# Performance work log

Hardware: AMD Instinct MI355X
Metric: run time of the kernel (lower is better)

## Reference

```python
import jax, jax.numpy as jnp
import numpy as np

B = 131072
F = 512

def setup_inputs() -> dict:
    key = jax.random.key(0)
    kx, kq = jax.random.split(key)
    x = jax.random.normal(kx, (B, F), dtype=jnp.float32)
    # Q param: xavier-normal init, then strictly-lower-triangular entries zeroed
    # (mask = tril(ones, diagonal=-1); Q.masked_fill_(mask, 0)).
    std = float(np.sqrt(2.0 / (F + F)))
    Q = jax.random.normal(kq, (F, F), dtype=jnp.float32) * std
    Q = jnp.triu(Q)  # zero strictly-lower triangle, keep diagonal
    return {"x": x, "Q": Q}

def reference(x, Q):
    # Original: diag(x @ Q @ x.T).view(-1, 1).
    # Equivalent per-row bilinear form, avoiding the [B, B] intermediate:
    # out[b] = sum_f sum_g x[b,f] Q[f,g] x[b,g]
    xQ = x @ Q                           # [B, F]
    out = jnp.sum(xQ * x, axis=1, keepdims=True)  # [B, 1]
    return out
```

## Files before the change

### kernel.cpp

```cpp
#include <hip/hip_runtime.h>
#include <hip/hip_bf16.h>

typedef __bf16 bf16_t;
typedef __bf16 bf16x8 __attribute__((ext_vector_type(8)));
typedef __bf16 bf16x4 __attribute__((ext_vector_type(4)));
typedef float f32x4 __attribute__((ext_vector_type(4)));

#define FDIM 512
#define BM 64
#define NTHR 512

__global__ void qtrans_kernel(const float* __restrict__ Q, bf16_t* __restrict__ Qt) {
    __shared__ float t[32][33];
    int tx = threadIdx.x & 31;
    int ty = threadIdx.x >> 5;
    int f0 = blockIdx.x * 32;
    int g0 = blockIdx.y * 32;
#pragma unroll
    for (int i = 0; i < 4; ++i)
        t[ty + 8 * i][tx] = Q[(size_t)(f0 + ty + 8 * i) * FDIM + g0 + tx];
    __syncthreads();
#pragma unroll
    for (int i = 0; i < 4; ++i)
        Qt[(size_t)(g0 + ty + 8 * i) * FDIM + f0 + tx] = (bf16_t)t[tx][ty + 8 * i];
}

__global__ __launch_bounds__(NTHR, 4) void bilinear_kernel(
    const float* __restrict__ x, const bf16_t* __restrict__ Qt,
    float* __restrict__ out)
{
    __shared__ bf16_t xs[BM * FDIM];
    __shared__ float rsum[8][BM];

    const int tid = threadIdx.x;
    const size_t blk = (size_t)blockIdx.x * BM;
    const float4* xin = (const float4*)(x + blk * FDIM);

#pragma unroll 1
    for (int it = 0; it < 4; ++it) {
        float4 vv[4];
#pragma unroll
        for (int j = 0; j < 4; ++j) vv[j] = xin[(it * 4 + j) * NTHR + tid];
#pragma unroll
        for (int j = 0; j < 4; ++j) {
            int e = ((it * 4 + j) * NTHR + tid) * 4;
            int row = e >> 9;
            int se = e ^ ((row & 7) << 3);
            bf16x4 b;
            b[0] = (bf16_t)vv[j].x; b[1] = (bf16_t)vv[j].y;
            b[2] = (bf16_t)vv[j].z; b[3] = (bf16_t)vv[j].w;
            *(bf16x4*)(xs + se) = b;
        }
        __builtin_amdgcn_sched_barrier(0);
    }
    __syncthreads();

    const int w   = tid >> 6;
    const int l   = tid & 63;
    const int col = l & 15;
    const int kg  = l >> 4;

    float rs[4][4];
#pragma unroll
    for (int m = 0; m < 4; ++m)
#pragma unroll
        for (int j = 0; j < 4; ++j) rs[m][j] = 0.0f;

#pragma unroll 1
    for (int pi = 0; pi < 4; ++pi) {
        const int p  = (pi < 2) ? w : (15 - w);
        const int h  = pi & 1;
        const int c0 = p * 32 + h * 16;
        const int nk = p + 1;

        f32x4 acc[4];
#pragma unroll
        for (int m = 0; m < 4; ++m)
#pragma unroll
            for (int j = 0; j < 4; ++j) acc[m][j] = 0.0f;

        const bf16_t* qb = Qt + (size_t)(c0 + col) * FDIM + kg * 8;
        bf16x8 b0 = *(const bf16x8*)(qb);

        for (int ks = 0; ks < nk; ++ks) {
            bf16x8 nb = b0;
            if (ks + 1 < nk) nb = *(const bf16x8*)(qb + (ks + 1) * 32);
            bf16x8 a[4];
#pragma unroll
            for (int m = 0; m < 4; ++m) {
                int r = m * 16 + col;
                int e = (r * FDIM + ks * 32 + kg * 8) ^ ((r & 7) << 3);
                a[m] = *(const bf16x8*)(xs + e);
            }
#pragma unroll
            for (int m = 0; m < 4; ++m)
                acc[m] = __builtin_amdgcn_mfma_f32_16x16x32_bf16(a[m], b0, acc[m], 0, 0, 0);
            b0 = nb;
        }

#pragma unroll
        for (int m = 0; m < 4; ++m) {
#pragma unroll
            for (int j = 0; j < 4; ++j) {
                int r = m * 16 + kg * 4 + j;
                int e = (r * FDIM + c0 + col) ^ ((r & 7) << 3);
                rs[m][j] += acc[m][j] * (float)xs[e];
            }
        }
    }

#pragma unroll
    for (int m = 0; m < 4; ++m) {
#pragma unroll
        for (int j = 0; j < 4; ++j) {
            float v2 = rs[m][j];
            v2 += __shfl_xor(v2, 1);
            v2 += __shfl_xor(v2, 2);
            v2 += __shfl_xor(v2, 4);
            v2 += __shfl_xor(v2, 8);
            rs[m][j] = v2;
        }
    }
    if (col == 0) {
#pragma unroll
        for (int m = 0; m < 4; ++m)
#pragma unroll
            for (int j = 0; j < 4; ++j)
                rsum[w][m * 16 + kg * 4 + j] = rs[m][j];
    }
    __syncthreads();

    if (tid < BM) {
        float s = 0.0f;
#pragma unroll
        for (int ww = 0; ww < 8; ++ww) s += rsum[ww][tid];
        out[blk + tid] = s;
    }
}

extern "C" void kernel_launch(void* const* d_in, const int* in_sizes, int n_in,
                              void* d_out, int out_size, void* d_ws, size_t ws_size,
                              hipStream_t stream) {
    const float* x = (const float*)d_in[0];
    const float* Q = (const float*)d_in[1];
    float* out = (float*)d_out;
    bf16_t* Qt = (bf16_t*)d_ws;

    const int B = in_sizes[0] / FDIM;

    dim3 tgrid(FDIM / 32, FDIM / 32);
    qtrans_kernel<<<tgrid, 256, 0, stream>>>(Q, Qt);
    bilinear_kernel<<<B / BM, NTHR, 0, stream>>>(x, Qt, out);
}
```

Before: 111.1 us.

## Make bilinear kernel persistent with register prefetch of next x tile

The launch changes from one block per 64-row tile to 512 persistent blocks that each loop over 4 tiles. During the MFMA compute of one tile, each block prefetches the next tile's x into registers in two halves, then writes it to shared memory after the reduction, so global loads overlap with compute. The LDS swizzle also widens from 8 to 16 rows to cut bank conflicts. In exchange, the hardcoded grid assumes B equals 512*4*64, and the extra registers may lower occupancy.

Result: slower. 220.3 us (+98.3%).

```diff
diff --git a/kernel.cpp b/kernel.cpp
--- a/kernel.cpp
+++ b/kernel.cpp
@@ -9,6 +9,8 @@
 #define FDIM 512
 #define BM 64
 #define NTHR 512
+#define NTILE 4
+#define NBLK 512
 
 __global__ void qtrans_kernel(const float* __restrict__ Q, bf16_t* __restrict__ Qt) {
     __shared__ float t[32][33];
@@ -33,108 +35,160 @@
     __shared__ float rsum[8][BM];
 
     const int tid = threadIdx.x;
-    const size_t blk = (size_t)blockIdx.x * BM;
-    const float4* xin = (const float4*)(x + blk * FDIM);
-
-#pragma unroll 1
-    for (int it = 0; it < 4; ++it) {
-        float4 vv[4];
-#pragma unroll
-        for (int j = 0; j < 4; ++j) vv[j] = xin[(it * 4 + j) * NTHR + tid];
-#pragma unroll
-        for (int j = 0; j < 4; ++j) {
-            int e = ((it * 4 + j) * NTHR + tid) * 4;
-            int row = e >> 9;
-            int se = e ^ ((row & 7) << 3);
-            bf16x4 b;
-            b[0] = (bf16_t)vv[j].x; b[1] = (bf16_t)vv[j].y;
-            b[2] = (bf16_t)vv[j].z; b[3] = (bf16_t)vv[j].w;
-            *(bf16x4*)(xs + se) = b;
-        }
-        __builtin_amdgcn_sched_barrier(0);
-    }
-    __syncthreads();
-
     const int w   = tid >> 6;
     const int l   = tid & 63;
     const int col = l & 15;
     const int kg  = l >> 4;
 
-    float rs[4][4];
-#pragma unroll
-    for (int m = 0; m < 4; ++m)
-#pragma unroll
-        for (int j = 0; j < 4; ++j) rs[m][j] = 0.0f;
-
+    {
+        const float4* xin = (const float4*)(x + (size_t)blockIdx.x * BM * FDIM);
 #pragma unroll 1
-    for (int pi = 0; pi < 4; ++pi) {
-        const int p  = (pi < 2) ? w : (15 - w);
-        const int h  = pi & 1;
-        const int c0 = p * 32 + h * 16;
-        const int nk = p + 1;
-
-        f32x4 acc[4];
-#pragma unroll
-        for (int m = 0; m < 4; ++m)
-#pragma unroll
-            for (int j = 0; j < 4; ++j) acc[m][j] = 0.0f;
-
-        const bf16_t* qb = Qt + (size_t)(c0 + col) * FDIM + kg * 8;
-        bf16x8 b0 = *(const bf16x8*)(qb);
-
-        for (int ks = 0; ks < nk; ++ks) {
-            bf16x8 nb = b0;
-            if (ks + 1 < nk) nb = *(const bf16x8*)(qb + (ks + 1) * 32);
-            bf16x8 a[4];
-#pragma unroll
-            for (int m = 0; m < 4; ++m) {
-                int r = m * 16 + col;
-                int e = (r * FDIM + ks * 32 + kg * 8) ^ ((r & 7) << 3);
-                a[m] = *(const bf16x8*)(xs + e);
-            }
-#pragma unroll
-            for (int m = 0; m < 4; ++m)
-                acc[m] = __builtin_amdgcn_mfma_f32_16x16x32_bf16(a[m], b0, acc[m], 0, 0, 0);
-            b0 = nb;
-        }
-
-#pragma unroll
-        for (int m = 0; m < 4; ++m) {
+        for (int it = 0; it < 4; ++it) {
+            float4 vv[4];
+#pragma unroll
+            for (int j = 0; j < 4; ++j) vv[j] = xin[(it * 4 + j) * NTHR + tid];
 #pragma unroll
             for (int j = 0; j < 4; ++j) {
-                int r = m * 16 + kg * 4 + j;
-                int e = (r * FDIM + c0 + col) ^ ((r & 7) << 3);
-                rs[m][j] += acc[m][j] * (float)xs[e];
-            }
-        }
-    }
-
-#pragma unroll
-    for (int m = 0; m < 4; ++m) {
-#pragma unroll
-        for (int j = 0; j < 4; ++j) {
-            float v2 = rs[m][j];
-            v2 += __shfl_xor(v2, 1);
-            v2 += __shfl_xor(v2, 2);
-            v2 += __shfl_xor(v2, 4);
-            v2 += __shfl_xor(v2, 8);
-            rs[m][j] = v2;
-        }
-    }
-    if (col == 0) {
-#pragma unroll
-        for (int m = 0; m < 4; ++m)
-#pragma unroll
-            for (int j = 0; j < 4; ++j)
-                rsum[w][m * 16 + kg * 4 + j] = rs[m][j];
+                int e = ((it * 4 + j) * NTHR + tid) * 4;
+                int row = e >> 9;
+                int se = e ^ ((row & 15) << 3);
+                bf16x4 b;
+                b[0] = (bf16_t)vv[j].x; b[1] = (bf16_t)vv[j].y;
+                b[2] = (bf16_t)vv[j].z; b[3] = (bf16_t)vv[j].w;
+                *(bf16x4*)(xs + se) = b;
+            }
+            __builtin_amdgcn_sched_barrier(0);
+        }
     }
     __syncthreads();
 
-    if (tid < BM) {
-        float s = 0.0f;
-#pragma unroll
-        for (int ww = 0; ww < 8; ++ww) s += rsum[ww][tid];
-        out[blk + tid] = s;
+#pragma unroll 1
+    for (int t = 0; t < NTILE; ++t) {
+        const size_t blk = ((size_t)t * NBLK + blockIdx.x) * BM;
+        const bool pf = (t + 1 < NTILE);
+        const float4* xnext = (const float4*)(x + (blk + (size_t)NBLK * BM) * FDIM);
+
+        float4 fA[8];
+        if (pf) {
+#pragma unroll
+            for (int j = 0; j < 8; ++j) fA[j] = xnext[j * NTHR + tid];
+        }
+        __builtin_amdgcn_sched_barrier(0);
+
+        float rs[4][4];
+#pragma unroll
+        for (int m = 0; m < 4; ++m)
+#pragma unroll
+            for (int j = 0; j < 4; ++j) rs[m][j] = 0.0f;
+
+        bf16x4 bA[8], bB[8];
+
+#pragma unroll 1
+        for (int pi = 0; pi < 4; ++pi) {
+            const int p  = (pi < 2) ? w : (15 - w);
+            const int h  = pi & 1;
+            const int c0 = p * 32 + h * 16;
+            const int nk = p + 1;
+
+            f32x4 acc[4];
+#pragma unroll
+            for (int m = 0; m < 4; ++m)
+#pragma unroll
+                for (int j = 0; j < 4; ++j) acc[m][j] = 0.0f;
+
+            const bf16_t* qb = Qt + (size_t)(c0 + col) * FDIM + kg * 8;
+            bf16x8 b0 = *(const bf16x8*)(qb);
+
+            for (int ks = 0; ks < nk; ++ks) {
+                bf16x8 nb = b0;
+                if (ks + 1 < nk) nb = *(const bf16x8*)(qb + (ks + 1) * 32);
+                bf16x8 a[4];
+#pragma unroll
+                for (int m = 0; m < 4; ++m) {
+                    int r = m * 16 + col;
+                    int e = (r * FDIM + ks * 32 + kg * 8) ^ ((r & 15) << 3);
+                    a[m] = *(const bf16x8*)(xs + e);
+                }
+#pragma unroll
+                for (int m = 0; m < 4; ++m)
+                    acc[m] = __builtin_amdgcn_mfma_f32_16x16x32_bf16(a[m], b0, acc[m], 0, 0, 0);
+                b0 = nb;
+            }
+
+#pragma unroll
+            for (int m = 0; m < 4; ++m) {
+#pragma unroll
+                for (int j = 0; j < 4; ++j) {
+                    int r = m * 16 + kg * 4 + j;
+                    int e = (r * FDIM + c0 + col) ^ ((r & 15) << 3);
+                    rs[m][j] += acc[m][j] * (float)xs[e];
+                }
+            }
+
+            if (pi == 1 && pf) {
+#pragma unroll
+                for (int j = 0; j < 8; ++j) {
+                    bA[j][0] = (bf16_t)fA[j].x; bA[j][1] = (bf16_t)fA[j].y;
+                    bA[j][2] = (bf16_t)fA[j].z; bA[j][3] = (bf16_t)fA[j].w;
+                }
+#pragma unroll
+                for (int j = 0; j < 8; ++j) fA[j] = xnext[(8 + j) * NTHR + tid];
+                __builtin_amdgcn_sched_barrier(0);
+            }
+            if (pi == 3 && pf) {
+#pragma unroll
+                for (int j = 0; j < 8; ++j) {
+                    bB[j][0] = (bf16_t)fA[j].x; bB[j][1] = (bf16_t)fA[j].y;
+                    bB[j][2] = (bf16_t)fA[j].z; bB[j][3] = (bf16_t)fA[j].w;
+                }
+            }
+        }
+
+#pragma unroll
+        for (int m = 0; m < 4; ++m) {
+#pragma unroll
+            for (int j = 0; j < 4; ++j) {
+                float v2 = rs[m][j];
+                v2 += __shfl_xor(v2, 1);
+                v2 += __shfl_xor(v2, 2);
+                v2 += __shfl_xor(v2, 4);
+                v2 += __shfl_xor(v2, 8);
+                rs[m][j] = v2;
+            }
+        }
+        if (col == 0) {
+#pragma unroll
+            for (int m = 0; m < 4; ++m)
+#pragma unroll
+                for (int j = 0; j < 4; ++j)
+                    rsum[w][m * 16 + kg * 4 + j] = rs[m][j];
+        }
+        __syncthreads();
+
+        if (tid < BM) {
+            float s = 0.0f;
+#pragma unroll
+            for (int ww = 0; ww < 8; ++ww) s += rsum[ww][tid];
+            out[blk + tid] = s;
+        }
+
+        if (pf) {
+#pragma unroll
+            for (int j = 0; j < 8; ++j) {
+                int e = (j * NTHR + tid) * 4;
+                int row = e >> 9;
+                int se = e ^ ((row & 15) << 3);
+                *(bf16x4*)(xs + se) = bA[j];
+            }
+#pragma unroll
+            for (int j = 0; j < 8; ++j) {
+                int e = ((8 + j) * NTHR + tid) * 4;
+                int row = e >> 9;
+                int se = e ^ ((row & 15) << 3);
+                *(bf16x4*)(xs + se) = bB[j];
+            }
+            __syncthreads();
+        }
     }
 }
 
@@ -146,9 +200,7 @@
     float* out = (float*)d_out;
     bf16_t* Qt = (bf16_t*)d_ws;
 
-    const int B = in_sizes[0] / FDIM;
-
     dim3 tgrid(FDIM / 32, FDIM / 32);
     qtrans_kernel<<<tgrid, 256, 0, stream>>>(Q, Qt);
-    bilinear_kernel<<<B / BM, NTHR, 0, stream>>>(x, Qt, out);
+    bilinear_kernel<<<NBLK, NTHR, 0, stream>>>(x, Qt, out);
 }
```

## Fuse column-tile loops so each A fragment feeds four MFMA accumulator sets

Applied to the files above, without the earlier changes.

Restructures the main compute loop so each wave processes all four of its column tiles (two triangular bands, two halves each) in one k-loop. Each x fragment read from LDS is reused across up to four B tiles instead of being reloaded per tile. The LDS XOR swizzle is widened from 8 to 16 rows to reduce bank conflicts under the new access pattern. In exchange it needs four times as many accumulator registers (64 floats), and the per-iteration band predicates add branching, which could lower occupancy under launch_bounds(512,4).

After: 112.4 us. About the same (+1.2%).

```diff
diff --git a/kernel.cpp b/kernel.cpp
--- a/kernel.cpp
+++ b/kernel.cpp
@@ -45,7 +45,7 @@
         for (int j = 0; j < 4; ++j) {
             int e = ((it * 4 + j) * NTHR + tid) * 4;
             int row = e >> 9;
-            int se = e ^ ((row & 7) << 3);
+            int se = e ^ ((row & 15) << 3);
             bf16x4 b;
             b[0] = (bf16_t)vv[j].x; b[1] = (bf16_t)vv[j].y;
             b[2] = (bf16_t)vv[j].z; b[3] = (bf16_t)vv[j].w;
@@ -60,51 +60,80 @@
     const int col = l & 15;
     const int kg  = l >> 4;
 
+    const int p0 = w;
+    const int p1 = 15 - w;
+
+    f32x4 acc[2][2][4];
+#pragma unroll
+    for (int pi = 0; pi < 2; ++pi)
+#pragma unroll
+        for (int h = 0; h < 2; ++h)
+#pragma unroll
+            for (int m = 0; m < 4; ++m)
+#pragma unroll
+                for (int j = 0; j < 4; ++j) acc[pi][h][m][j] = 0.0f;
+
+    const bf16_t* qp[2][2];
+#pragma unroll
+    for (int pi = 0; pi < 2; ++pi) {
+        int p = pi ? p1 : p0;
+#pragma unroll
+        for (int h = 0; h < 2; ++h)
+            qp[pi][h] = Qt + (size_t)(p * 32 + h * 16 + col) * FDIM + kg * 8;
+    }
+
+    int rbase[4];
+#pragma unroll
+    for (int m = 0; m < 4; ++m) rbase[m] = (m * 16 + col) * FDIM + kg * 8;
+    const int amask = col << 3;
+
+#pragma unroll 1
+    for (int ks = 0; ks < 16; ++ks) {
+        bf16x8 a[4];
+#pragma unroll
+        for (int m = 0; m < 4; ++m)
+            a[m] = *(const bf16x8*)(xs + ((rbase[m] + ks * 32) ^ amask));
+
+        if (ks <= p0) {
+#pragma unroll
+            for (int h = 0; h < 2; ++h) {
+                bf16x8 b = *(const bf16x8*)(qp[0][h] + ks * 32);
+#pragma unroll
+                for (int m = 0; m < 4; ++m)
+                    acc[0][h][m] = __builtin_amdgcn_mfma_f32_16x16x32_bf16(a[m], b, acc[0][h][m], 0, 0, 0);
+            }
+        }
+        if (ks <= p1) {
+#pragma unroll
+            for (int h = 0; h < 2; ++h) {
+                bf16x8 b = *(const bf16x8*)(qp[1][h] + ks * 32);
+#pragma unroll
+                for (int m = 0; m < 4; ++m)
+                    acc[1][h][m] = __builtin_amdgcn_mfma_f32_16x16x32_bf16(a[m], b, acc[1][h][m], 0, 0, 0);
+            }
+        }
+    }
+
     float rs[4][4];
 #pragma unroll
     for (int m = 0; m < 4; ++m)
 #pragma unroll
         for (int j = 0; j < 4; ++j) rs[m][j] = 0.0f;
 
-#pragma unroll 1
-    for (int pi = 0; pi < 4; ++pi) {
-        const int p  = (pi < 2) ? w : (15 - w);
-        const int h  = pi & 1;
-        const int c0 = p * 32 + h * 16;
-        const int nk = p + 1;
-
-        f32x4 acc[4];
 #pragma unroll
-        for (int m = 0; m < 4; ++m)
+    for (int pi = 0; pi < 2; ++pi) {
+        const int p = pi ? p1 : p0;
 #pragma unroll
-            for (int j = 0; j < 4; ++j) acc[m][j] = 0.0f;
-
-        const bf16_t* qb = Qt + (size_t)(c0 + col) * FDIM + kg * 8;
-        bf16x8 b0 = *(const bf16x8*)(qb);
-
-        for (int ks = 0; ks < nk; ++ks) {
-            bf16x8 nb = b0;
-            if (ks + 1 < nk) nb = *(const bf16x8*)(qb + (ks + 1) * 32);
-            bf16x8 a[4];
+        for (int h = 0; h < 2; ++h) {
+            const int c0 = p * 32 + h * 16;
 #pragma unroll
             for (int m = 0; m < 4; ++m) {
-                int r = m * 16 + col;
-                int e = (r * FDIM + ks * 32 + kg * 8) ^ ((r & 7) << 3);
-                a[m] = *(const bf16x8*)(xs + e);
-            }
 #pragma unroll
-            for (int m = 0; m < 4; ++m)
-                acc[m] = __builtin_amdgcn_mfma_f32_16x16x32_bf16(a[m], b0, acc[m], 0, 0, 0);
-            b0 = nb;
-        }
-
-#pragma unroll
-        for (int m = 0; m < 4; ++m) {
-#pragma unroll
-            for (int j = 0; j < 4; ++j) {
-                int r = m * 16 + kg * 4 + j;
-                int e = (r * FDIM + c0 + col) ^ ((r & 7) << 3);
-                rs[m][j] += acc[m][j] * (float)xs[e];
+                for (int j = 0; j < 4; ++j) {
+                    int r = m * 16 + kg * 4 + j;
+                    int e = (r * FDIM + c0 + col) ^ ((r & 15) << 3);
+                    rs[m][j] += acc[pi][h][m][j] * (float)xs[e];
+                }
             }
         }
     }
```

## Keep x rows in registers and stream Q panels through double-buffered LDS

Applied to the files above, without the earlier changes.

Each wave now loads its 16 rows of x straight from global memory into registers as bf16 MFMA A-fragments, instead of staging the 64-row x tile in LDS. Q^T is streamed in 32-column panels through double-buffered shared memory, loading only the upper-triangular part each panel needs. Each block covers 128 rows, so per-wave reduction happens with shuffles only and needs no cross-wave LDS sum. This removes the large x LDS tile and the per-block re-reading of Q from global memory. In exchange it uses many more registers, puts a barrier on every panel, and re-reads fp32 x from global for the epilogue dot product. The grid is fixed at 1024 blocks, which hardcodes B.

After: 122.0 us. 9.8% more time.

```diff
diff --git a/kernel.cpp b/kernel.cpp
--- a/kernel.cpp
+++ b/kernel.cpp
@@ -7,8 +7,9 @@
 typedef float f32x4 __attribute__((ext_vector_type(4)));
 
 #define FDIM 512
-#define BM 64
 #define NTHR 512
+#define BROWS 128
+#define NBLK 1024
 
 __global__ void qtrans_kernel(const float* __restrict__ Q, bf16_t* __restrict__ Qt) {
     __shared__ float t[32][33];
@@ -29,112 +30,106 @@
     const float* __restrict__ x, const bf16_t* __restrict__ Qt,
     float* __restrict__ out)
 {
-    __shared__ bf16_t xs[BM * FDIM];
-    __shared__ float rsum[8][BM];
+    __shared__ bf16_t panel[2][32 * FDIM];
 
     const int tid = threadIdx.x;
-    const size_t blk = (size_t)blockIdx.x * BM;
-    const float4* xin = (const float4*)(x + blk * FDIM);
-
-#pragma unroll 1
-    for (int it = 0; it < 4; ++it) {
-        float4 vv[4];
-#pragma unroll
-        for (int j = 0; j < 4; ++j) vv[j] = xin[(it * 4 + j) * NTHR + tid];
-#pragma unroll
-        for (int j = 0; j < 4; ++j) {
-            int e = ((it * 4 + j) * NTHR + tid) * 4;
-            int row = e >> 9;
-            int se = e ^ ((row & 7) << 3);
-            bf16x4 b;
-            b[0] = (bf16_t)vv[j].x; b[1] = (bf16_t)vv[j].y;
-            b[2] = (bf16_t)vv[j].z; b[3] = (bf16_t)vv[j].w;
-            *(bf16x4*)(xs + se) = b;
-        }
-        __builtin_amdgcn_sched_barrier(0);
-    }
-    __syncthreads();
-
     const int w   = tid >> 6;
     const int l   = tid & 63;
     const int col = l & 15;
     const int kg  = l >> 4;
 
-    float rs[4][4];
+    const int row0w = blockIdx.x * BROWS + w * 16;
+
+    const float* arow = x + (size_t)(row0w + col) * FDIM + kg * 8;
+    bf16x8 a[16];
 #pragma unroll
-    for (int m = 0; m < 4; ++m)
+    for (int ks = 0; ks < 16; ++ks) {
+        float4 f0 = *(const float4*)(arow + ks * 32);
+        float4 f1 = *(const float4*)(arow + ks * 32 + 4);
+        bf16x8 v;
+        v[0] = (bf16_t)f0.x; v[1] = (bf16_t)f0.y; v[2] = (bf16_t)f0.z; v[3] = (bf16_t)f0.w;
+        v[4] = (bf16_t)f1.x; v[5] = (bf16_t)f1.y; v[6] = (bf16_t)f1.z; v[7] = (bf16_t)f1.w;
+        a[ks] = v;
+        if ((ks & 3) == 3) __builtin_amdgcn_sched_barrier(0);
+    }
+
+    {
+        const int c = w;
 #pragma unroll
-        for (int j = 0; j < 4; ++j) rs[m][j] = 0.0f;
+        for (int i = 0; i < 4; ++i) {
+            int cc = i * 8 + w;
+            if (l < 4) {
+                bf16x8 q = *(const bf16x8*)(Qt + (size_t)cc * FDIM + l * 8);
+                int e = cc * FDIM + ((l * 8) ^ ((cc & 15) << 3));
+                *(bf16x8*)(&panel[0][0] + e) = q;
+            }
+        }
+        (void)c;
+    }
+    __syncthreads();
+
+    float rs[4] = {0.f, 0.f, 0.f, 0.f};
 
 #pragma unroll 1
-    for (int pi = 0; pi < 4; ++pi) {
-        const int p  = (pi < 2) ? w : (15 - w);
-        const int h  = pi & 1;
-        const int c0 = p * 32 + h * 16;
-        const int nk = p + 1;
+    for (int p = 0; p < 16; ++p) {
+        const int buf = p & 1;
+        const bf16_t* pb = &panel[buf][0];
 
-        f32x4 acc[4];
+        if (p + 1 < 16) {
+            const int pn = p + 1;
+            const int lim = 4 * (pn + 1);
+            bf16_t* pw = &panel[buf ^ 1][0];
 #pragma unroll
-        for (int m = 0; m < 4; ++m)
-#pragma unroll
-            for (int j = 0; j < 4; ++j) acc[m][j] = 0.0f;
-
-        const bf16_t* qb = Qt + (size_t)(c0 + col) * FDIM + kg * 8;
-        bf16x8 b0 = *(const bf16x8*)(qb);
-
-        for (int ks = 0; ks < nk; ++ks) {
-            bf16x8 nb = b0;
-            if (ks + 1 < nk) nb = *(const bf16x8*)(qb + (ks + 1) * 32);
-            bf16x8 a[4];
-#pragma unroll
-            for (int m = 0; m < 4; ++m) {
-                int r = m * 16 + col;
-                int e = (r * FDIM + ks * 32 + kg * 8) ^ ((r & 7) << 3);
-                a[m] = *(const bf16x8*)(xs + e);
+            for (int i = 0; i < 4; ++i) {
+                int cc = i * 8 + w;
+                if (l < lim) {
+                    bf16x8 q = *(const bf16x8*)(Qt + (size_t)(pn * 32 + cc) * FDIM + l * 8);
+                    int e = cc * FDIM + ((l * 8) ^ ((cc & 15) << 3));
+                    *(bf16x8*)(pw + e) = q;
+                }
             }
-#pragma unroll
-            for (int m = 0; m < 4; ++m)
-                acc[m] = __builtin_amdgcn_mfma_f32_16x16x32_bf16(a[m], b0, acc[m], 0, 0, 0);
-            b0 = nb;
         }
 
+        f32x4 acc0, acc1;
 #pragma unroll
-        for (int m = 0; m < 4; ++m) {
+        for (int j = 0; j < 4; ++j) { acc0[j] = 0.f; acc1[j] = 0.f; }
+
+        const int kswz = col << 3;
 #pragma unroll
-            for (int j = 0; j < 4; ++j) {
-                int r = m * 16 + kg * 4 + j;
-                int e = (r * FDIM + c0 + col) ^ ((r & 7) << 3);
-                rs[m][j] += acc[m][j] * (float)xs[e];
+        for (int ks = 0; ks < 16; ++ks) {
+            if (ks <= p) {
+                int kk = (ks * 32 + kg * 8) ^ kswz;
+                bf16x8 b0 = *(const bf16x8*)(pb + col * FDIM + kk);
+                bf16x8 b1 = *(const bf16x8*)(pb + (16 + col) * FDIM + kk);
+                acc0 = __builtin_amdgcn_mfma_f32_16x16x32_bf16(a[ks], b0, acc0, 0, 0, 0);
+                acc1 = __builtin_amdgcn_mfma_f32_16x16x32_bf16(a[ks], b1, acc1, 0, 0, 0);
             }
         }
+
+        const float* xe = x + (size_t)(row0w + kg * 4) * FDIM + p * 32 + col;
+#pragma unroll
+        for (int j = 0; j < 4; ++j) {
+            float e0 = xe[(size_t)j * FDIM];
+            float e1 = xe[(size_t)j * FDIM + 16];
+            rs[j] += acc0[j] * e0 + acc1[j] * e1;
+        }
+
+        __syncthreads();
     }
 
 #pragma unroll
-    for (int m = 0; m < 4; ++m) {
-#pragma unroll
-        for (int j = 0; j < 4; ++j) {
-            float v2 = rs[m][j];
-            v2 += __shfl_xor(v2, 1);
-            v2 += __shfl_xor(v2, 2);
-            v2 += __shfl_xor(v2, 4);
-            v2 += __shfl_xor(v2, 8);
-            rs[m][j] = v2;
-        }
+    for (int j = 0; j < 4; ++j) {
+        float v2 = rs[j];
+        v2 += __shfl_xor(v2, 1);
+        v2 += __shfl_xor(v2, 2);
+        v2 += __shfl_xor(v2, 4);
+        v2 += __shfl_xor(v2, 8);
+        rs[j] = v2;
     }
     if (col == 0) {
 #pragma unroll
-        for (int m = 0; m < 4; ++m)
-#pragma unroll
-            for (int j = 0; j < 4; ++j)
-                rsum[w][m * 16 + kg * 4 + j] = rs[m][j];
-    }
-    __syncthreads();
-
-    if (tid < BM) {
-        float s = 0.0f;
-#pragma unroll
-        for (int ww = 0; ww < 8; ++ww) s += rsum[ww][tid];
-        out[blk + tid] = s;
+        for (int j = 0; j < 4; ++j)
+            out[row0w + kg * 4 + j] = rs[j];
     }
 }
 
@@ -146,9 +141,7 @@
     float* out = (float*)d_out;
     bf16_t* Qt = (bf16_t*)d_ws;
 
-    const int B = in_sizes[0] / FDIM;
-
     dim3 tgrid(FDIM / 32, FDIM / 32);
     qtrans_kernel<<<tgrid, 256, 0, stream>>>(Q, Qt);
-    bilinear_kernel<<<B / BM, NTHR, 0, stream>>>(x, Qt, out);
+    bilinear_kernel<<<NBLK, NTHR, 0, stream>>>(x, Qt, out);
 }
```
